# Optimization experiments

Hardware: AMD Instinct MI355X
Metric: run time of the kernel (lower is better)

## Reference

```python
import jax, jax.numpy as jnp
import numpy as np

N = 100000   # nodes
E = 600000   # edges
G = 64       # graphs in batch
H = 128      # hidden size
F_NODE = 2
F_EDGE = 7
RH = 500     # reghead size
NEG_SLOPE = 0.01
BN_EPS = 1e-5


def leaky(x):
    return jnp.where(x >= 0, x, NEG_SLOPE * x)


def gine_conv(x, src, dst, edge_attr, edge_W, edge_b, W1, b1, gamma, beta, W2, b2):
    # PyG GINEConv: message = ReLU(x_j + Lin(edge_attr)); sum-aggregate at dst;
    # out = nn((1+eps)*x + aggr) with eps=0; nn = Lin -> BN(train) -> LeakyReLU -> Lin -> LeakyReLU
    e = edge_attr @ edge_W.T + edge_b                 # [E, d_in]
    m = jax.nn.relu(x[src] + e)                       # gather + add + relu
    aggr = jax.ops.segment_sum(m, dst, num_segments=N)
    h = x + aggr
    h = h @ W1.T + b1                                 # [N, H]
    mu = jnp.mean(h, axis=0)
    var = jnp.var(h, axis=0)                          # biased, matches BN training
    h = gamma * (h - mu) * jax.lax.rsqrt(var + BN_EPS) + beta
    h = leaky(h)
    h = h @ W2.T + b2
    return leaky(h)


def setup_inputs() -> dict:
    key = jax.random.key(0)
    ks = jax.random.split(key, 24)

    def lin(k, out_d, in_d):
        s = 1.0 / np.sqrt(in_d)
        k1, k2 = jax.random.split(k)
        return (jax.random.uniform(k1, (out_d, in_d), jnp.float32, -s, s),
                jax.random.uniform(k2, (out_d,), jnp.float32, -s, s))

    x = jax.random.normal(ks[0], (N, F_NODE), jnp.float32)
    edge_index = jax.random.randint(ks[1], (2, E), 0, N, jnp.int32)
    batch = jnp.sort(jax.random.randint(ks[2], (N,), 0, G, jnp.int32))
    edge_attr = jax.random.normal(ks[3], (E, F_EDGE), jnp.float32)

    # layer 0 (in_dim = F_NODE)
    ew0, eb0 = lin(ks[4], F_NODE, F_EDGE)
    w10, b10 = lin(ks[5], H, F_NODE)
    g0, be0 = jnp.ones((H,), jnp.float32), jnp.zeros((H,), jnp.float32)
    w20, b20 = lin(ks[6], H, H)

    # 3 hidden layers, stacked (in_dim = H)
    L = 3
    ewS = jnp.stack([lin(ks[7 + i], H, F_EDGE)[0] for i in range(L)])
    ebS = jnp.stack([lin(jax.random.fold_in(ks[7 + i], 1), H, F_EDGE)[1] for i in range(L)])
    w1S = jnp.stack([lin(ks[10 + i], H, H)[0] for i in range(L)])
    b1S = jnp.stack([lin(jax.random.fold_in(ks[10 + i], 1), H, H)[1] for i in range(L)])
    gS = jnp.ones((L, H), jnp.float32)
    beS = jnp.zeros((L, H), jnp.float32)
    w2S = jnp.stack([lin(ks[13 + i], H, H)[0] for i in range(L)])
    b2S = jnp.stack([lin(jax.random.fold_in(ks[13 + i], 1), H, H)[1] for i in range(L)])

    wr, br = lin(ks[16], RH, H)
    we, be_ = lin(ks[17], 1, RH)

    return {"x": x, "edge_index": edge_index, "batch": batch, "edge_attr": edge_attr,
            "ew0": ew0, "eb0": eb0, "w10": w10, "b10": b10, "g0": g0, "be0": be0,
            "w20": w20, "b20": b20,
            "ewS": ewS, "ebS": ebS, "w1S": w1S, "b1S": b1S, "gS": gS, "beS": beS,
            "w2S": w2S, "b2S": b2S, "wr": wr, "br": br, "we": we, "be_": be_}


def reference(x, edge_index, batch, edge_attr,
              ew0, eb0, w10, b10, g0, be0, w20, b20,
              ewS, ebS, w1S, b1S, gS, beS, w2S, b2S,
              wr, br, we, be_):
    src, dst = edge_index[0], edge_index[1]
    h = gine_conv(x, src, dst, edge_attr, ew0, eb0, w10, b10, g0, be0, w20, b20)
    h = leaky(h)  # outer self.relu; dropout p=0 is identity
    for i in range(ewS.shape[0]):
        h = gine_conv(h, src, dst, edge_attr, ewS[i], ebS[i], w1S[i], b1S[i],
                      gS[i], beS[i], w2S[i], b2S[i])
        h = leaky(h)
    # global_mean_pool
    sums = jax.ops.segment_sum(h, batch, num_segments=G)
    cnt = jax.ops.segment_sum(jnp.ones((h.shape[0],), h.dtype), batch, num_segments=G)
    pooled = sums / jnp.maximum(cnt, 1.0)[:, None]
    # reghead_layers == 2
    r = leaky(pooled @ wr.T + br)
    return r @ we.T + be_
```

## Files before the change

kernel.cpp:

```cpp
#include <hip/hip_runtime.h>

#define NNODES 100000
#define NEDGES 600000
#define NGRAPH 64
#define HID 128
#define RHD 500
#define NB ((NNODES + 255) / 256)
#define EB ((NEDGES + 255) / 256)
#define GG ((NNODES + 63) / 64)

typedef __attribute__((ext_vector_type(8))) short short8;
typedef __attribute__((ext_vector_type(4))) float f32x4;

__device__ __forceinline__ float leaky1(float x) { return x >= 0.0f ? x : 0.01f * x; }

__device__ __forceinline__ void splitf(float a, unsigned short& h, unsigned short& l)
{
    unsigned u = __float_as_uint(a);
    unsigned r = (u + 0x7FFFu + ((u >> 16) & 1u)) & 0xFFFF0000u;
    h = (unsigned short)(r >> 16);
    float res = a - __uint_as_float(r);
    unsigned u2 = __float_as_uint(res);
    l = (unsigned short)((u2 + 0x7FFFu + ((u2 >> 16) & 1u)) >> 16);
}

__global__ __launch_bounds__(256) void hist_kernel(
    const int* __restrict__ ei, int* __restrict__ deg)
{
    int e = blockIdx.x * 256 + threadIdx.x;
    if (e < NEDGES) atomicAdd(&deg[ei[NEDGES + e]], 1);
}

__global__ __launch_bounds__(256) void scan_blk(
    const int* __restrict__ deg, int* __restrict__ incl, int* __restrict__ bsum)
{
    __shared__ int s[256];
    int t = threadIdx.x;
    int n = blockIdx.x * 256 + t;
    int v = (n < NNODES) ? deg[n] : 0;
    int x = v;
    s[t] = x;
    __syncthreads();
    for (int off = 1; off < 256; off <<= 1) {
        int y = (t >= off) ? s[t - off] : 0;
        __syncthreads();
        x += y; s[t] = x;
        __syncthreads();
    }
    if (n < NNODES) incl[n] = x;
    if (t == 255) bsum[blockIdx.x] = x;
}

__global__ __launch_bounds__(512) void scan_bsum(int* __restrict__ bsum, int nblk)
{
    __shared__ int s[512];
    int t = threadIdx.x;
    int v = (t < nblk) ? bsum[t] : 0;
    int x = v;
    s[t] = x;
    __syncthreads();
    for (int off = 1; off < 512; off <<= 1) {
        int y = (t >= off) ? s[t - off] : 0;
        __syncthreads();
        x += y; s[t] = x;
        __syncthreads();
    }
    if (t < nblk) bsum[t] = x - v;
}

__global__ __launch_bounds__(256) void finalize_rp(
    const int* __restrict__ deg, const int* __restrict__ bsum,
    int* __restrict__ rp, int* __restrict__ cursor)
{
    int n = blockIdx.x * 256 + threadIdx.x;
    if (n >= NNODES) return;
    int ig = rp[n] + bsum[blockIdx.x];
    int st = ig - deg[n];
    rp[n] = st;
    cursor[n] = st;
    if (n == NNODES - 1) rp[NNODES] = ig;
}

__global__ __launch_bounds__(256) void scatter_kernel(
    const int* __restrict__ ei, int* __restrict__ cursor, int* __restrict__ eid)
{
    int e = blockIdx.x * 256 + threadIdx.x;
    if (e >= NEDGES) return;
    int d = ei[NEDGES + e];
    int pos = atomicAdd(&cursor[d], 1);
    eid[pos] = e;
}

__global__ __launch_bounds__(256) void seg_sort(
    const int* __restrict__ rp, int* __restrict__ eid)
{
    int n = blockIdx.x * 256 + threadIdx.x;
    if (n >= NNODES) return;
    int beg = rp[n], end = rp[n + 1];
    for (int i = beg + 1; i < end; ++i) {
        int key = eid[i];
        int j = i - 1;
        while (j >= beg && eid[j] > key) { eid[j + 1] = eid[j]; --j; }
        eid[j + 1] = key;
    }
}

__global__ __launch_bounds__(256) void permute_kernel(
    const int* __restrict__ eid, const int* __restrict__ ei,
    const float* __restrict__ ea, int* __restrict__ srcp, float* __restrict__ eap)
{
    int p = blockIdx.x * 256 + threadIdx.x;
    if (p >= NEDGES) return;
    int id = eid[p];
    srcp[p] = ei[id];
    const float* s = ea + (size_t)id * 7;
    float* d = eap + (size_t)p * 7;
#pragma unroll
    for (int k = 0; k < 7; ++k) d[k] = s[k];
}

__global__ __launch_bounds__(256) void wsplit_kernel(
    const float* __restrict__ w, unsigned short* __restrict__ wh,
    unsigned short* __restrict__ wl)
{
    int i = blockIdx.x * 256 + threadIdx.x;
    unsigned short h, l;
    splitf(w[i], h, l);
    wh[i] = h;
    wl[i] = l;
}

__global__ __launch_bounds__(256) void aggregate0_kernel(
    const float* __restrict__ x, const int* __restrict__ rp,
    const int* __restrict__ srcp, const float* __restrict__ eap,
    const float* __restrict__ ew, const float* __restrict__ eb,
    float* __restrict__ aggr2)
{
    int n = blockIdx.x * 256 + threadIdx.x;
    if (n >= NNODES) return;
    float w0[7], w1[7];
#pragma unroll
    for (int k = 0; k < 7; ++k) { w0[k] = ew[k]; w1[k] = ew[7 + k]; }
    float e0b = eb[0], e1b = eb[1];
    float a0 = x[n * 2 + 0], a1 = x[n * 2 + 1];
    int beg = rp[n], end = rp[n + 1];
    for (int e = beg; e < end; ++e) {
        int s = srcp[e];
        const float* ap = eap + (size_t)e * 7;
        float t0 = e0b, t1 = e1b;
#pragma unroll
        for (int k = 0; k < 7; ++k) {
            float av = ap[k];
            t0 = fmaf(av, w0[k], t0);
            t1 = fmaf(av, w1[k], t1);
        }
        a0 += fmaxf(x[s * 2 + 0] + t0, 0.0f);
        a1 += fmaxf(x[s * 2 + 1] + t1, 0.0f);
    }
    aggr2[n * 2 + 0] = a0;
    aggr2[n * 2 + 1] = a1;
}

__global__ __launch_bounds__(256) void aggregate_kernel(
    const float* __restrict__ hin, const int* __restrict__ rp,
    const int* __restrict__ srcp, const float* __restrict__ eap,
    const float* __restrict__ ew, const float* __restrict__ eb,
    float* __restrict__ A)
{
    int lane = threadIdx.x & 63;
    int w = threadIdx.x >> 6;
    int nbase = blockIdx.x * 32 + w * 8;
    float ew0[7], ew1[7];
#pragma unroll
    for (int k = 0; k < 7; ++k) {
        ew0[k] = ew[lane * 7 + k];
        ew1[k] = ew[(lane + 64) * 7 + k];
    }
    float eb0v = eb[lane], eb1v = eb[lane + 64];
    for (int n = nbase; n < nbase + 8; ++n) {
        float a0 = hin[(size_t)n * HID + lane];
        float a1 = hin[(size_t)n * HID + 64 + lane];
        int beg = rp[n], end = rp[n + 1];
        for (int e = beg; e < end; ++e) {
            int s = srcp[e];
            const float* ap = eap + (size_t)e * 7;
            float t0 = eb0v, t1 = eb1v;
#pragma unroll
            for (int k = 0; k < 7; ++k) {
                float av = ap[k];
                t0 = fmaf(av, ew0[k], t0);
                t1 = fmaf(av, ew1[k], t1);
            }
            float x0 = hin[(size_t)s * HID + lane];
            float x1 = hin[(size_t)s * HID + 64 + lane];
            a0 += fmaxf(x0 + t0, 0.0f);
            a1 += fmaxf(x1 + t1, 0.0f);
        }
        float* Ap = A + (size_t)n * HID;
        Ap[lane] = a0;
        Ap[64 + lane] = a1;
    }
}

__global__ __launch_bounds__(256) void gemm1_l0_kernel(
    const float* __restrict__ aggr2,
    const float* __restrict__ w1, const float* __restrict__ b1,
    float* __restrict__ h1)
{
    int n = blockIdx.x * 256 + threadIdx.x;
    if (n >= NNODES) return;
    float x0 = aggr2[n * 2 + 0];
    float x1 = aggr2[n * 2 + 1];
    float4* out4 = (float4*)(h1 + (size_t)n * HID);
    for (int j = 0; j < HID; j += 4) {
        float4 o;
        o.x = fmaf(x1, w1[(j + 0) * 2 + 1], fmaf(x0, w1[(j + 0) * 2 + 0], b1[j + 0]));
        o.y = fmaf(x1, w1[(j + 1) * 2 + 1], fmaf(x0, w1[(j + 1) * 2 + 0], b1[j + 1]));
        o.z = fmaf(x1, w1[(j + 2) * 2 + 1], fmaf(x0, w1[(j + 2) * 2 + 0], b1[j + 2]));
        o.w = fmaf(x1, w1[(j + 3) * 2 + 1], fmaf(x0, w1[(j + 3) * 2 + 0], b1[j + 3]));
        out4[j >> 2] = o;
    }
}

__global__ __launch_bounds__(256) void bn_stats_part(
    const float* __restrict__ h1, float* __restrict__ part)
{
    __shared__ float ls[HID], lq[HID];
    int c = threadIdx.x & 127;
    int half = threadIdx.x >> 7;
    int base = blockIdx.x * 256;
    int end = base + 256; if (end > NNODES) end = NNODES;
    float s = 0.0f, q = 0.0f;
    for (int r = base + half; r < end; r += 2) {
        float v = h1[(size_t)r * HID + c];
        s += v;
        q = fmaf(v, v, q);
    }
    if (half) { ls[c] = s; lq[c] = q; }
    __syncthreads();
    if (!half) {
        s += ls[c]; q += lq[c];
        part[(size_t)blockIdx.x * 256 + c] = s;
        part[(size_t)blockIdx.x * 256 + 128 + c] = q;
    }
}

__global__ __launch_bounds__(64) void bn_finalize(
    const float* __restrict__ part, int nblk,
    const float* __restrict__ gamma, const float* __restrict__ beta,
    float* __restrict__ scsh)
{
    int c = blockIdx.x;
    int lane = threadIdx.x;
    float s = 0.0f, q = 0.0f;
    for (int i = lane; i < nblk; i += 64) {
        s += part[(size_t)i * 256 + c];
        q += part[(size_t)i * 256 + 128 + c];
    }
#pragma unroll
    for (int off = 32; off >= 1; off >>= 1) {
        s += __shfl_down(s, off);
        q += __shfl_down(q, off);
    }
    if (lane == 0) {
        const float invN = 1.0f / (float)NNODES;
        float mu = s * invN;
        float var = fmaf(-mu, mu, q * invN);
        float iv = rsqrtf(var + 1e-5f);
        float sc = gamma[c] * iv;
        scsh[c] = sc;
        scsh[HID + c] = beta[c] - mu * sc;
    }
}

template<int PRE, int POST>
__global__ __launch_bounds__(256) void gemm_mfma(
    const float* __restrict__ Ain, const float* __restrict__ scsh,
    const unsigned short* __restrict__ wh, const unsigned short* __restrict__ wl,
    const float* __restrict__ bias, float* __restrict__ Hout)
{
    __shared__ __align__(16) short lds[16384];
    const int t = threadIdx.x;
    const int mb = blockIdx.x * 64;

    const float4* sc4 = (const float4*)scsh;
    const float4* sh4 = (const float4*)(scsh + HID);

#pragma unroll
    for (int u = 0; u < 4; ++u) {
        int idx = u * 256 + t;
        int row = idx >> 4, sl = idx & 15;
        float4 v0 = make_float4(0.f, 0.f, 0.f, 0.f);
        float4 v1 = make_float4(0.f, 0.f, 0.f, 0.f);
        int gr = mb + row;
        if (gr < NNODES) {
            const float4* p = (const float4*)(Ain + (size_t)gr * HID + sl * 8);
            v0 = p[0]; v1 = p[1];
            if (PRE) {
                float4 c0 = sc4[sl * 2], c1 = sc4[sl * 2 + 1];
                float4 s0 = sh4[sl * 2], s1 = sh4[sl * 2 + 1];
                v0.x = leaky1(fmaf(v0.x, c0.x, s0.x));
                v0.y = leaky1(fmaf(v0.y, c0.y, s0.y));
                v0.z = leaky1(fmaf(v0.z, c0.z, s0.z));
                v0.w = leaky1(fmaf(v0.w, c0.w, s0.w));
                v1.x = leaky1(fmaf(v1.x, c1.x, s1.x));
                v1.y = leaky1(fmaf(v1.y, c1.y, s1.y));
                v1.z = leaky1(fmaf(v1.z, c1.z, s1.z));
                v1.w = leaky1(fmaf(v1.w, c1.w, s1.w));
            }
        }
        unsigned short h[8], l[8];
        splitf(v0.x, h[0], l[0]); splitf(v0.y, h[1], l[1]);
        splitf(v0.z, h[2], l[2]); splitf(v0.w, h[3], l[3]);
        splitf(v1.x, h[4], l[4]); splitf(v1.y, h[5], l[5]);
        splitf(v1.z, h[6], l[6]); splitf(v1.w, h[7], l[7]);
        short8 hv, lv;
#pragma unroll
        for (int e = 0; e < 8; ++e) { hv[e] = (short)h[e]; lv[e] = (short)l[e]; }
        int byt = row * 256 + ((sl ^ (row & 7)) << 4);
        *(short8*)((char*)lds + byt) = hv;
        *(short8*)((char*)lds + 16384 + byt) = lv;
    }
    __syncthreads();

    const int lane = t & 63;
    const int wv = t >> 6;
    const int cl = lane & 15, g = lane >> 4, x = lane & 7;
    const int colbase = wv * 32;

    int aoff[4];
#pragma unroll
    for (int ks = 0; ks < 4; ++ks)
        aoff[ks] = cl * 256 + (((ks * 4 + g) ^ x) << 4);

    const unsigned short* wb_h0 = wh + (size_t)(colbase + cl) * HID + g * 8;
    const unsigned short* wb_h1 = wb_h0 + 16 * HID;
    const unsigned short* wb_l0 = wl + (size_t)(colbase + cl) * HID + g * 8;
    const unsigned short* wb_l1 = wb_l0 + 16 * HID;

    f32x4 acc[4][2];
#pragma unroll
    for (int rt = 0; rt < 4; ++rt) {
        acc[rt][0] = (f32x4){0.f, 0.f, 0.f, 0.f};
        acc[rt][1] = (f32x4){0.f, 0.f, 0.f, 0.f};
    }

#pragma unroll
    for (int ks = 0; ks < 4; ++ks) {
        short8 bh0 = *(const short8*)(wb_h0 + ks * 32);
        short8 bh1 = *(const short8*)(wb_h1 + ks * 32);
        short8 bl0 = *(const short8*)(wb_l0 + ks * 32);
        short8 bl1 = *(const short8*)(wb_l1 + ks * 32);
#pragma unroll
        for (int rt = 0; rt < 4; ++rt) {
            short8 ah = *(const short8*)((const char*)lds + (rt * 4096) + aoff[ks]);
            short8 al = *(const short8*)((const char*)lds + (16384 + rt * 4096) + aoff[ks]);
            acc[rt][0] = __builtin_amdgcn_mfma_f32_16x16x32_bf16(ah, bh0, acc[rt][0], 0, 0, 0);
            acc[rt][1] = __builtin_amdgcn_mfma_f32_16x16x32_bf16(ah, bh1, acc[rt][1], 0, 0, 0);
            acc[rt][0] = __builtin_amdgcn_mfma_f32_16x16x32_bf16(al, bh0, acc[rt][0], 0, 0, 0);
            acc[rt][1] = __builtin_amdgcn_mfma_f32_16x16x32_bf16(al, bh1, acc[rt][1], 0, 0, 0);
            acc[rt][0] = __builtin_amdgcn_mfma_f32_16x16x32_bf16(ah, bl0, acc[rt][0], 0, 0, 0);
            acc[rt][1] = __builtin_amdgcn_mfma_f32_16x16x32_bf16(ah, bl1, acc[rt][1], 0, 0, 0);
        }
    }

    float bj0 = bias[colbase + cl];
    float bj1 = bias[colbase + 16 + cl];
#pragma unroll
    for (int rt = 0; rt < 4; ++rt) {
        int rbase = mb + rt * 16 + g * 4;
#pragma unroll
        for (int r = 0; r < 4; ++r) {
            int grow = rbase + r;
            if (grow < NNODES) {
                float o0 = acc[rt][0][r] + bj0;
                float o1 = acc[rt][1][r] + bj1;
                if (POST) { o0 = leaky1(leaky1(o0)); o1 = leaky1(leaky1(o1)); }
                Hout[(size_t)grow * HID + colbase + cl] = o0;
                Hout[(size_t)grow * HID + colbase + 16 + cl] = o1;
            }
        }
    }
}

__global__ __launch_bounds__(256) void pool_kernel(
    const float* __restrict__ h, const int* __restrict__ batch,
    float* __restrict__ sums, float* __restrict__ cnt)
{
    int c = threadIdx.x & 127;
    int half = threadIdx.x >> 7;
    int base = blockIdx.x * 128 + half * 64;
    if (base >= NNODES) return;
    int end = base + 64; if (end > NNODES) end = NNODES;
    int g = batch[base];
    float acc = 0.0f, k = 0.0f;
    for (int n = base; n < end; ++n) {
        int gn = batch[n];
        if (gn != g) {
            atomicAdd(&sums[g * HID + c], acc);
            if (c == 0) atomicAdd(&cnt[g], k);
            acc = 0.0f; k = 0.0f; g = gn;
        }
        acc += h[(size_t)n * HID + c];
        k += 1.0f;
    }
    atomicAdd(&sums[g * HID + c], acc);
    if (c == 0) atomicAdd(&cnt[g], k);
}

__global__ __launch_bounds__(512) void reghead_kernel(
    const float* __restrict__ sums, const float* __restrict__ cnt,
    const float* __restrict__ wr, const float* __restrict__ br,
    const float* __restrict__ we, const float* __restrict__ be,
    float* __restrict__ out)
{
    __shared__ float pool[8 * HID];
    __shared__ float red[8][8];
    int g0 = blockIdx.x * 8;
    for (int i = threadIdx.x; i < 8 * HID; i += 512) {
        int g = g0 + (i >> 7);
        float c = cnt[g]; c = fmaxf(c, 1.0f);
        pool[i] = sums[g * HID + (i & 127)] / c;
    }
    __syncthreads();
    int j = threadIdx.x;
    float p[8];
#pragma unroll
    for (int g = 0; g < 8; ++g) p[g] = 0.0f;
    if (j < RHD) {
        float accs[8];
        float bjv = br[j];
#pragma unroll
        for (int g = 0; g < 8; ++g) accs[g] = bjv;
        const float4* wr4 = (const float4*)(wr + (size_t)j * HID);
        const float4* pool4 = (const float4*)pool;
        for (int k = 0; k < 32; ++k) {
            float4 w = wr4[k];
#pragma unroll
            for (int g = 0; g < 8; ++g) {
                float4 pv = pool4[g * 32 + k];
                accs[g] = fmaf(w.x, pv.x, accs[g]);
                accs[g] = fmaf(w.y, pv.y, accs[g]);
                accs[g] = fmaf(w.z, pv.z, accs[g]);
                accs[g] = fmaf(w.w, pv.w, accs[g]);
            }
        }
        float wej = we[j];
#pragma unroll
        for (int g = 0; g < 8; ++g) p[g] = leaky1(accs[g]) * wej;
    }
    int lane = threadIdx.x & 63, wid = threadIdx.x >> 6;
#pragma unroll
    for (int g = 0; g < 8; ++g) {
        float v = p[g];
        v += __shfl_down(v, 32); v += __shfl_down(v, 16); v += __shfl_down(v, 8);
        v += __shfl_down(v, 4);  v += __shfl_down(v, 2);  v += __shfl_down(v, 1);
        if (lane == 0) red[g][wid] = v;
    }
    __syncthreads();
    if (threadIdx.x < 8) {
        float sv = be[0];
#pragma unroll
        for (int w = 0; w < 8; ++w) sv += red[threadIdx.x][w];
        out[g0 + threadIdx.x] = sv;
    }
}

extern "C" void kernel_launch(void* const* d_in, const int* in_sizes, int n_in,
                              void* d_out, int out_size, void* d_ws, size_t ws_size,
                              hipStream_t stream)
{
    const float* x     = (const float*)d_in[0];
    const int*   ei    = (const int*)d_in[1];
    const int*   batch = (const int*)d_in[2];
    const float* ea    = (const float*)d_in[3];
    const float* ew0   = (const float*)d_in[4];
    const float* eb0   = (const float*)d_in[5];
    const float* w10   = (const float*)d_in[6];
    const float* b10   = (const float*)d_in[7];
    const float* g0v   = (const float*)d_in[8];
    const float* be0   = (const float*)d_in[9];
    const float* w20   = (const float*)d_in[10];
    const float* b20   = (const float*)d_in[11];
    const float* ewS   = (const float*)d_in[12];
    const float* ebS   = (const float*)d_in[13];
    const float* w1S   = (const float*)d_in[14];
    const float* b1S   = (const float*)d_in[15];
    const float* gS    = (const float*)d_in[16];
    const float* beS   = (const float*)d_in[17];
    const float* w2S   = (const float*)d_in[18];
    const float* b2S   = (const float*)d_in[19];
    const float* wr    = (const float*)d_in[20];
    const float* br    = (const float*)d_in[21];
    const float* we    = (const float*)d_in[22];
    const float* be_   = (const float*)d_in[23];

    float* ws    = (float*)d_ws;
    float* buf0  = ws;
    float* buf1  = buf0 + (size_t)NNODES * HID;
    float* part  = buf1 + (size_t)NNODES * HID;
    float* scsh  = part + (size_t)NB * 256;
    float* sums  = scsh + 256;
    float* cnt   = sums + NGRAPH * HID;
    float* aggr2 = cnt + NGRAPH;
    float* eap   = aggr2 + (size_t)NNODES * 2;
    int*   deg    = (int*)(eap + (size_t)NEDGES * 7);
    int*   cursor = deg + NNODES;
    int*   bsum   = cursor + NNODES;
    int*   rp     = bsum + 512;
    int*   eid    = rp + NNODES + 1;
    int*   srcp   = eid + NEDGES;
    unsigned short* whA = (unsigned short*)(srcp + NEDGES);
    unsigned short* wlA = whA + 7 * 16384;
    float* out   = (float*)d_out;

    hipMemsetAsync(deg, 0, (size_t)NNODES * sizeof(int), stream);
    hist_kernel<<<EB, 256, 0, stream>>>(ei, deg);
    scan_blk<<<NB, 256, 0, stream>>>(deg, rp, bsum);
    scan_bsum<<<1, 512, 0, stream>>>(bsum, NB);
    finalize_rp<<<NB, 256, 0, stream>>>(deg, bsum, rp, cursor);
    scatter_kernel<<<EB, 256, 0, stream>>>(ei, cursor, eid);
    seg_sort<<<NB, 256, 0, stream>>>(rp, eid);
    permute_kernel<<<EB, 256, 0, stream>>>(eid, ei, ea, srcp, eap);

    wsplit_kernel<<<64, 256, 0, stream>>>(w20, whA, wlA);
    for (int i = 0; i < 3; ++i) {
        wsplit_kernel<<<64, 256, 0, stream>>>(w1S + (size_t)i * HID * HID,
            whA + (size_t)(1 + i) * 16384, wlA + (size_t)(1 + i) * 16384);
        wsplit_kernel<<<64, 256, 0, stream>>>(w2S + (size_t)i * HID * HID,
            whA + (size_t)(4 + i) * 16384, wlA + (size_t)(4 + i) * 16384);
    }

    aggregate0_kernel<<<NB, 256, 0, stream>>>(x, rp, srcp, eap, ew0, eb0, aggr2);
    gemm1_l0_kernel<<<NB, 256, 0, stream>>>(aggr2, w10, b10, buf0);
    bn_stats_part<<<NB, 256, 0, stream>>>(buf0, part);
    bn_finalize<<<HID, 64, 0, stream>>>(part, NB, g0v, be0, scsh);
    gemm_mfma<1, 1><<<GG, 256, 0, stream>>>(buf0, scsh, whA, wlA, b20, buf1);

    int cur = 1;
    float* bufs[2] = { buf0, buf1 };
    for (int i = 0; i < 3; ++i) {
        float* hin  = bufs[cur];
        float* hoth = bufs[cur ^ 1];
        aggregate_kernel<<<NNODES / 32, 256, 0, stream>>>(hin, rp, srcp, eap,
            ewS + (size_t)i * HID * 7, ebS + (size_t)i * HID, hoth);
        gemm_mfma<0, 0><<<GG, 256, 0, stream>>>(hoth, scsh,
            whA + (size_t)(1 + i) * 16384, wlA + (size_t)(1 + i) * 16384,
            b1S + (size_t)i * HID, hin);
        bn_stats_part<<<NB, 256, 0, stream>>>(hin, part);
        bn_finalize<<<HID, 64, 0, stream>>>(part, NB,
            gS + (size_t)i * HID, beS + (size_t)i * HID, scsh);
        gemm_mfma<1, 1><<<GG, 256, 0, stream>>>(hin, scsh,
            whA + (size_t)(4 + i) * 16384, wlA + (size_t)(4 + i) * 16384,
            b2S + (size_t)i * HID, hoth);
        cur ^= 1;
    }

    hipMemsetAsync(sums, 0, (size_t)(NGRAPH * HID + NGRAPH) * sizeof(float), stream);
    pool_kernel<<<(NNODES + 127) / 128, 256, 0, stream>>>(bufs[cur], batch, sums, cnt);
    reghead_kernel<<<NGRAPH / 8, 512, 0, stream>>>(sums, cnt, wr, br, we, be_, out);
}
```

Measured before the change: 827.7 us.

## Fuse edge aggregation, first MFMA GEMM and BN partial stats per layer

Merges the hidden-layer aggregation kernel, the first split-bf16 MFMA GEMM and the BN partial-statistics kernel into one kernel. Aggregated rows are split into hi/lo bf16 and written straight into LDS, then multiplied with MFMA, and per-column sum and sum-of-squares are reduced in-block. This removes the round trip of the aggregate buffer and the reread of h1 for statistics, plus two launches per layer. In exchange, each block of 64 rows runs the irregular gather with 4 waves (16 rows each), which lowers the parallelism of the gather phase relative to the old 32-rows-per-block launch.

```diff
diff --git a/kernel.cpp b/kernel.cpp
--- a/kernel.cpp
+++ b/kernel.cpp
@@ -159,47 +159,6 @@
     }
     aggr2[n * 2 + 0] = a0;
     aggr2[n * 2 + 1] = a1;
-}
-
-__global__ __launch_bounds__(256) void aggregate_kernel(
-    const float* __restrict__ hin, const int* __restrict__ rp,
-    const int* __restrict__ srcp, const float* __restrict__ eap,
-    const float* __restrict__ ew, const float* __restrict__ eb,
-    float* __restrict__ A)
-{
-    int lane = threadIdx.x & 63;
-    int w = threadIdx.x >> 6;
-    int nbase = blockIdx.x * 32 + w * 8;
-    float ew0[7], ew1[7];
-#pragma unroll
-    for (int k = 0; k < 7; ++k) {
-        ew0[k] = ew[lane * 7 + k];
-        ew1[k] = ew[(lane + 64) * 7 + k];
-    }
-    float eb0v = eb[lane], eb1v = eb[lane + 64];
-    for (int n = nbase; n < nbase + 8; ++n) {
-        float a0 = hin[(size_t)n * HID + lane];
-        float a1 = hin[(size_t)n * HID + 64 + lane];
-        int beg = rp[n], end = rp[n + 1];
-        for (int e = beg; e < end; ++e) {
-            int s = srcp[e];
-            const float* ap = eap + (size_t)e * 7;
-            float t0 = eb0v, t1 = eb1v;
-#pragma unroll
-            for (int k = 0; k < 7; ++k) {
-                float av = ap[k];
-                t0 = fmaf(av, ew0[k], t0);
-                t1 = fmaf(av, ew1[k], t1);
-            }
-            float x0 = hin[(size_t)s * HID + lane];
-            float x1 = hin[(size_t)s * HID + 64 + lane];
-            a0 += fmaxf(x0 + t0, 0.0f);
-            a1 += fmaxf(x1 + t1, 0.0f);
-        }
-        float* Ap = A + (size_t)n * HID;
-        Ap[lane] = a0;
-        Ap[64 + lane] = a1;
-    }
 }
 
 __global__ __launch_bounds__(256) void gemm1_l0_kernel(
@@ -270,6 +229,139 @@
         float sc = gamma[c] * iv;
         scsh[c] = sc;
         scsh[HID + c] = beta[c] - mu * sc;
+    }
+}
+
+__global__ __launch_bounds__(256) void agg_gemm1(
+    const float* __restrict__ hin, const int* __restrict__ rp,
+    const int* __restrict__ srcp, const float* __restrict__ eap,
+    const float* __restrict__ ew, const float* __restrict__ eb,
+    const unsigned short* __restrict__ wh, const unsigned short* __restrict__ wl,
+    const float* __restrict__ b1, float* __restrict__ h1,
+    float* __restrict__ part)
+{
+    __shared__ __align__(16) short lds[16384];
+    const int t = threadIdx.x;
+    const int lane = t & 63;
+    const int wv = t >> 6;
+    const int mb = blockIdx.x * 64;
+
+    float ew0[7], ew1[7];
+#pragma unroll
+    for (int k = 0; k < 7; ++k) {
+        ew0[k] = ew[lane * 7 + k];
+        ew1[k] = ew[(lane + 64) * 7 + k];
+    }
+    float eb0v = eb[lane], eb1v = eb[lane + 64];
+    const int slot0 = lane >> 3, slot1 = 8 + (lane >> 3);
+    const int lb = (lane & 7) * 2;
+
+    for (int rr = 0; rr < 16; ++rr) {
+        int row = wv * 16 + rr;
+        int gr = mb + row;
+        float a0 = 0.0f, a1 = 0.0f;
+        if (gr < NNODES) {
+            a0 = hin[(size_t)gr * HID + lane];
+            a1 = hin[(size_t)gr * HID + 64 + lane];
+            int beg = rp[gr], end = rp[gr + 1];
+            for (int e = beg; e < end; ++e) {
+                int s = srcp[e];
+                const float* ap = eap + (size_t)e * 7;
+                float t0 = eb0v, t1 = eb1v;
+#pragma unroll
+                for (int k = 0; k < 7; ++k) {
+                    float av = ap[k];
+                    t0 = fmaf(av, ew0[k], t0);
+                    t1 = fmaf(av, ew1[k], t1);
+                }
+                float x0 = hin[(size_t)s * HID + lane];
+                float x1 = hin[(size_t)s * HID + 64 + lane];
+                a0 += fmaxf(x0 + t0, 0.0f);
+                a1 += fmaxf(x1 + t1, 0.0f);
+            }
+        }
+        unsigned short h0, l0, h1v, l1v;
+        splitf(a0, h0, l0);
+        splitf(a1, h1v, l1v);
+        int rsw = row & 7;
+        int b0 = row * 256 + ((slot0 ^ rsw) << 4) + lb;
+        int b1b = row * 256 + ((slot1 ^ rsw) << 4) + lb;
+        *(short*)((char*)lds + b0) = (short)h0;
+        *(short*)((char*)lds + b1b) = (short)h1v;
+        *(short*)((char*)lds + 16384 + b0) = (short)l0;
+        *(short*)((char*)lds + 16384 + b1b) = (short)l1v;
+    }
+    __syncthreads();
+
+    const int cl = lane & 15, g = lane >> 4, x = lane & 7;
+    const int colbase = wv * 32;
+
+    int aoff[4];
+#pragma unroll
+    for (int ks = 0; ks < 4; ++ks)
+        aoff[ks] = cl * 256 + (((ks * 4 + g) ^ x) << 4);
+
+    const unsigned short* wb_h0 = wh + (size_t)(colbase + cl) * HID + g * 8;
+    const unsigned short* wb_h1 = wb_h0 + 16 * HID;
+    const unsigned short* wb_l0 = wl + (size_t)(colbase + cl) * HID + g * 8;
+    const unsigned short* wb_l1 = wb_l0 + 16 * HID;
+
+    f32x4 acc[4][2];
+#pragma unroll
+    for (int rt = 0; rt < 4; ++rt) {
+        acc[rt][0] = (f32x4){0.f, 0.f, 0.f, 0.f};
+        acc[rt][1] = (f32x4){0.f, 0.f, 0.f, 0.f};
+    }
+
+#pragma unroll
+    for (int ks = 0; ks < 4; ++ks) {
+        short8 bh0 = *(const short8*)(wb_h0 + ks * 32);
+        short8 bh1 = *(const short8*)(wb_h1 + ks * 32);
+        short8 bl0 = *(const short8*)(wb_l0 + ks * 32);
+        short8 bl1 = *(const short8*)(wb_l1 + ks * 32);
+#pragma unroll
+        for (int rt = 0; rt < 4; ++rt) {
+            short8 ah = *(const short8*)((const char*)lds + (rt * 4096) + aoff[ks]);
+            short8 al = *(const short8*)((const char*)lds + (16384 + rt * 4096) + aoff[ks]);
+            acc[rt][0] = __builtin_amdgcn_mfma_f32_16x16x32_bf16(ah, bh0, acc[rt][0], 0, 0, 0);
+            acc[rt][1] = __builtin_amdgcn_mfma_f32_16x16x32_bf16(ah, bh1, acc[rt][1], 0, 0, 0);
+            acc[rt][0] = __builtin_amdgcn_mfma_f32_16x16x32_bf16(al, bh0, acc[rt][0], 0, 0, 0);
+            acc[rt][1] = __builtin_amdgcn_mfma_f32_16x16x32_bf16(al, bh1, acc[rt][1], 0, 0, 0);
+            acc[rt][0] = __builtin_amdgcn_mfma_f32_16x16x32_bf16(ah, bl0, acc[rt][0], 0, 0, 0);
+            acc[rt][1] = __builtin_amdgcn_mfma_f32_16x16x32_bf16(ah, bl1, acc[rt][1], 0, 0, 0);
+        }
+    }
+
+    float bj0 = b1[colbase + cl];
+    float bj1 = b1[colbase + 16 + cl];
+    float s0 = 0.f, q0 = 0.f, s1 = 0.f, q1 = 0.f;
+#pragma unroll
+    for (int rt = 0; rt < 4; ++rt) {
+        int rbase = mb + rt * 16 + g * 4;
+#pragma unroll
+        for (int r = 0; r < 4; ++r) {
+            int grow = rbase + r;
+            if (grow < NNODES) {
+                float o0 = acc[rt][0][r] + bj0;
+                float o1 = acc[rt][1][r] + bj1;
+                h1[(size_t)grow * HID + colbase + cl] = o0;
+                h1[(size_t)grow * HID + colbase + 16 + cl] = o1;
+                s0 += o0; q0 = fmaf(o0, o0, q0);
+                s1 += o1; q1 = fmaf(o1, o1, q1);
+            }
+        }
+    }
+    __syncthreads();
+    float* red = (float*)lds;
+    red[(colbase + cl) * 4 + g] = s0;
+    red[(colbase + 16 + cl) * 4 + g] = s1;
+    red[512 + (colbase + cl) * 4 + g] = q0;
+    red[512 + (colbase + 16 + cl) * 4 + g] = q1;
+    __syncthreads();
+    {
+        int stat = t >> 7, col = t & 127;
+        const float* bp = red + stat * 512 + col * 4;
+        part[(size_t)blockIdx.x * 256 + stat * 128 + col] = bp[0] + bp[1] + bp[2] + bp[3];
     }
 }
 
@@ -499,7 +591,7 @@
     float* buf0  = ws;
     float* buf1  = buf0 + (size_t)NNODES * HID;
     float* part  = buf1 + (size_t)NNODES * HID;
-    float* scsh  = part + (size_t)NB * 256;
+    float* scsh  = part + (size_t)GG * 256;
     float* sums  = scsh + 256;
     float* cnt   = sums + NGRAPH * HID;
     float* aggr2 = cnt + NGRAPH;
@@ -537,26 +629,19 @@
     bn_finalize<<<HID, 64, 0, stream>>>(part, NB, g0v, be0, scsh);
     gemm_mfma<1, 1><<<GG, 256, 0, stream>>>(buf0, scsh, whA, wlA, b20, buf1);
 
-    int cur = 1;
-    float* bufs[2] = { buf0, buf1 };
     for (int i = 0; i < 3; ++i) {
-        float* hin  = bufs[cur];
-        float* hoth = bufs[cur ^ 1];
-        aggregate_kernel<<<NNODES / 32, 256, 0, stream>>>(hin, rp, srcp, eap,
-            ewS + (size_t)i * HID * 7, ebS + (size_t)i * HID, hoth);
-        gemm_mfma<0, 0><<<GG, 256, 0, stream>>>(hoth, scsh,
+        agg_gemm1<<<GG, 256, 0, stream>>>(buf1, rp, srcp, eap,
+            ewS + (size_t)i * HID * 7, ebS + (size_t)i * HID,
             whA + (size_t)(1 + i) * 16384, wlA + (size_t)(1 + i) * 16384,
-            b1S + (size_t)i * HID, hin);
-        bn_stats_part<<<NB, 256, 0, stream>>>(hin, part);
-        bn_finalize<<<HID, 64, 0, stream>>>(part, NB,
+            b1S + (size_t)i * HID, buf0, part);
+        bn_finalize<<<HID, 64, 0, stream>>>(part, GG,
             gS + (size_t)i * HID, beS + (size_t)i * HID, scsh);
-        gemm_mfma<1, 1><<<GG, 256, 0, stream>>>(hin, scsh,
+        gemm_mfma<1, 1><<<GG, 256, 0, stream>>>(buf0, scsh,
             whA + (size_t)(4 + i) * 16384, wlA + (size_t)(4 + i) * 16384,
-            b2S + (size_t)i * HID, hoth);
-        cur ^= 1;
+            b2S + (size_t)i * HID, buf1);
     }
 
     hipMemsetAsync(sums, 0, (size_t)(NGRAPH * HID + NGRAPH) * sizeof(float), stream);
-    pool_kernel<<<(NNODES + 127) / 128, 256, 0, stream>>>(bufs[cur], batch, sums, cnt);
+    pool_kernel<<<(NNODES + 127) / 128, 256, 0, stream>>>(buf1, batch, sums, cnt);
     reghead_kernel<<<NGRAPH / 8, 512, 0, stream>>>(sums, cnt, wr, br, we, be_, out);
 }
```

Result: slower. 879.8 us (+6.3%).
